# Kernel tuning notes

Measured on AMD Instinct MI355X. Metric: run time of the kernel, lower is better.

The kernel has to match this reference:

```python
import jax, jax.numpy as jnp
import numpy as np
from jax import lax

STRIDE, HID, LAT, R, LVL, SCALE = 8, 128, 64, 3, 4, 4
FF = 50 * 60  # frame_flow spatial size


def bilinear_sample(img, x, y):
    # img: [Q,C,H,W]; x,y: [Q,P] float pixel coords; zero outside image. -> [Q,C,P]
    Q, C, H, W = img.shape
    x0 = jnp.floor(x); y0 = jnp.floor(y)
    wx = x - x0; wy = y - y0
    flat = img.reshape(Q, C, H * W)
    def g(ix, iy):
        valid = (ix >= 0) & (ix <= W - 1) & (iy >= 0) & (iy <= H - 1)
        idx = (jnp.clip(iy, 0, H - 1).astype(jnp.int32) * W
               + jnp.clip(ix, 0, W - 1).astype(jnp.int32))[:, None, :]
        v = jnp.take_along_axis(flat, jnp.broadcast_to(idx, (Q, C, x.shape[-1])), axis=2)
        return v * valid[:, None, :]
    return (g(x0, y0) * ((1 - wy) * (1 - wx))[:, None, :]
            + g(x0 + 1, y0) * ((1 - wy) * wx)[:, None, :]
            + g(x0, y0 + 1) * (wy * (1 - wx))[:, None, :]
            + g(x0 + 1, y0 + 1) * (wy * wx)[:, None, :])


def resize_bilinear(img, oh, ow, align_corners):
    # img: [Q,C,H,W] -> [Q,C,oh,ow], matches F.interpolate(mode='bilinear')
    Q, C, H, W = img.shape
    def coords(o, i):
        if align_corners:
            return jnp.linspace(0.0, i - 1.0, o)
        return jnp.clip((jnp.arange(o) + 0.5) * (i / o) - 0.5, 0.0, i - 1.0)
    ys, xs = coords(oh, H), coords(ow, W)
    y0 = jnp.floor(ys).astype(jnp.int32); y1 = jnp.minimum(y0 + 1, H - 1); wy = ys - y0
    x0 = jnp.floor(xs).astype(jnp.int32); x1 = jnp.minimum(x0 + 1, W - 1); wx = xs - x0
    v = jnp.take(img, y0, axis=2) * (1 - wy)[:, None] + jnp.take(img, y1, axis=2) * wy[:, None]
    return jnp.take(v, x0, axis=3) * (1 - wx) + jnp.take(v, x1, axis=3) * wx


def avg_pool2(x):
    return lax.reduce_window(x, 0.0, lax.add, (1, 1, 2, 2), (1, 1, 2, 2), 'VALID') * 0.25


def encode(x, w, stride):
    # patchify conv + instance-norm (surrogate for BasicEncoder, same in/out shapes)
    y = lax.conv_general_dilated(x, w, (stride, stride), 'VALID',
                                 dimension_numbers=('NCHW', 'OIHW', 'NCHW'))
    m = y.mean(axis=(2, 3), keepdims=True)
    v = y.var(axis=(2, 3), keepdims=True)
    return (y - m) * lax.rsqrt(v + 1e-5)


def build_pyramid(fmaps):
    # fmaps: [B,S,C,H,W] -> list of [B*S,C,Hl,Wl] (CorrBlock.__init__)
    B, S, C, H, W = fmaps.shape
    x = fmaps.reshape(B * S, C, H, W)
    pyr = [x]
    for _ in range(LVL - 1):
        x = avg_pool2(x)
        pyr.append(x)
    return pyr


def corr_pyramid(pyr, feats):
    # feats: [B,S,N,C] -> list of [B*S,N,Hl,Wl] (CorrBlock.corr)
    B, S, N, C = feats.shape
    f = feats.reshape(B * S, N, C)
    scale = 1.0 / jnp.sqrt(jnp.float32(C))
    return [jnp.einsum('qnc,qchw->qnhw', f, p) * scale for p in pyr]


def corr_sample(corrs, coords):
    # CorrBlock.sample: bilinear gather of (2R+1)^2 window per level at coords/2^lvl
    B, S, N, _ = coords.shape
    d = jnp.arange(-R, R + 1, dtype=coords.dtype)
    dy, dx = jnp.meshgrid(d, d, indexing='ij')
    dx = dx.reshape(1, -1); dy = dy.reshape(1, -1)
    out = []
    for i, c in enumerate(corrs):
        H, W = c.shape[-2:]
        cen = coords.reshape(B * S * N, 1, 2) / (2.0 ** i)
        x = cen[..., 0] + dx; y = cen[..., 1] + dy  # [BSN,K]
        v = bilinear_sample(c.reshape(B * S * N, 1, H, W), x, y)
        out.append(v.reshape(B, S, N, -1))
    return jnp.concatenate(out, axis=-1)  # [B,S,N,LVL*(2R+1)^2]


def flows_from(coords):
    B, S, N, _ = coords.shape
    f = (coords[:, 1:] - coords[:, :-1]).transpose(0, 2, 1, 3).reshape(B * N, S - 1, 2)
    return jnp.concatenate([f, f[:, -1:]], axis=1)


def delta_block(fc, fl, ff, xy, w1, b1, w2, b2):
    # surrogate for DeltaBlock / DeltaBlock_temp: MLP over concatenated context
    h = jnp.concatenate([fc, fl, ff, xy], axis=-1)
    return jax.nn.relu(h @ w1 + b1) @ w2 + b2  # [B*N,S,2]


def forward_model(rgbs, points_0, fnet_w, fnet_fine_w, linear_w, linear_b,
                  dbs_w1, dbs_b1, dbs_w2, dbs_b2,
                  dbt_w1, dbt_b1, dbt_w2, dbt_b2, iters):
    B, S, C, H, W = rgbs.shape
    N = points_0.shape[1]
    rgbs = 2.0 * (rgbs / 255.0) - 1.0
    rgbs_ = rgbs.reshape(B * S, C, H, W)
    # frame_flow context (assumes B==1, like the torch code): [N,S,3000]
    ff = jnp.concatenate([rgbs_[-1:, 0], rgbs_[1:, 0] - rgbs_[:-1, 0]], axis=0)[:, None]
    ff = resize_bilinear(ff, 50, 60, False).reshape(1, S, FF)
    frame_flow = jnp.broadcast_to(ff, (N, S, FF))

    # ---- initialize_ : coarse stage (stride 8) ----
    Hc, Wc = H // STRIDE, W // STRIDE
    fmaps_c = encode(rgbs_, fnet_w, STRIDE).reshape(B, S, LAT, Hc, Wc)
    coords = jnp.broadcast_to((points_0 / float(STRIDE))[:, None], (B, S, N, 2))
    f0 = bilinear_sample(fmaps_c[:, 0], coords[:, 0, :, 0], coords[:, 0, :, 1]).transpose(0, 2, 1)
    feats = jnp.broadcast_to(f0[:, None], (B, S, N, LAT))
    xys0_c = jnp.broadcast_to(coords[:, 0].transpose(1, 0, 2), (N, S, 2))
    coords = lax.stop_gradient(coords)
    corrs_c = corr_pyramid(build_pyramid(fmaps_c), feats)
    fc = [resize_bilinear(c, 14, 14, True).reshape(B, S, N, 196) for c in corrs_c]
    fcorrs_ = jnp.stack(fc).mean(0).transpose(0, 2, 1, 3).reshape(B * N, S, 196)
    delta = delta_block(fcorrs_, flows_from(coords), frame_flow, xys0_c,
                        dbs_w1, dbs_b1, dbs_w2, dbs_b2)
    coords = coords + delta.reshape(B, N, S, 2).transpose(0, 2, 1, 3)
    coords_init = coords * float(STRIDE)

    # ---- fine refinement (stride 2), iterative ----
    fs = STRIDE // SCALE  # 2
    Hf, Wf = H // fs, W // fs
    fmaps = encode(rgbs_, fnet_fine_w, fs).reshape(B, S, LAT, Hf, Wf)
    coords = coords_init / float(fs)
    pyr = build_pyramid(fmaps)
    f0 = bilinear_sample(fmaps[:, 0], coords[:, 0, :, 0], coords[:, 0, :, 1]).transpose(0, 2, 1)
    corrs1 = corr_pyramid(pyr, jnp.broadcast_to(f0[:, None], (B, S, N, LAT)))
    xys0 = jnp.broadcast_to(coords[:, 0].transpose(1, 0, 2), (N, S, 2))
    inds2 = jnp.clip(jnp.arange(S) - 2, 0, None)
    inds4 = jnp.clip(jnp.arange(S) - 4, 0, None)
    preds = [coords_init]
    for _ in range(iters):
        coords = lax.stop_gradient(coords)
        def shifted_feats(inds, coords=coords):
            fm = fmaps[:, inds].reshape(B * S, LAT, Hf, Wf)
            co = coords[:, inds].reshape(B * S, N, 2)
            return bilinear_sample(fm, co[..., 0], co[..., 1]).transpose(0, 2, 1).reshape(B, S, N, LAT)
        corrs2 = corr_pyramid(pyr, shifted_feats(inds2))
        corrs4 = corr_pyramid(pyr, shifted_feats(inds4))
        def bn(f):
            return f.transpose(0, 2, 1, 3).reshape(B * N, S, -1)
        fcorrs_ = jnp.concatenate([bn(corr_sample(corrs1, coords)),
                                   bn(corr_sample(corrs2, coords)),
                                   bn(corr_sample(corrs4, coords))], axis=2)
        fcorrs_ = fcorrs_ @ linear_w + linear_b  # 588 -> 392
        delta = delta_block(fcorrs_, flows_from(coords), frame_flow, xys0,
                            dbt_w1, dbt_b1, dbt_w2, dbt_b2)
        coords = coords + delta.reshape(B, N, S, 2).transpose(0, 2, 1, 3)
        preds.append(coords * float(fs))
    return jnp.stack(preds)  # [iters+1, B, S, N, 2]


def setup_inputs():
    ks = jax.random.split(jax.random.key(0), 12)
    B, S, N, H, W = 1, 16, 64, 200, 240
    rgbs = jax.random.uniform(ks[0], (B, S, 1, H, W), jnp.float32) * 255.0
    points_0 = jax.random.uniform(ks[1], (B, N, 2), jnp.float32) * jnp.array([W - 1.0, H - 1.0], jnp.float32)
    d_sp, d_tp = 196 + 2 + FF + 2, 392 + 2 + FF + 2
    return {
        'rgbs': rgbs, 'points_0': points_0,
        'fnet_w': jax.random.normal(ks[2], (LAT, 1, STRIDE, STRIDE), jnp.float32) * 0.1,
        'fnet_fine_w': jax.random.normal(ks[3], (LAT, 1, 2, 2), jnp.float32) * 0.3,
        'linear_w': jax.random.normal(ks[4], (588, 392), jnp.float32) / np.sqrt(588.0).astype(np.float32),
        'linear_b': jnp.zeros((392,), jnp.float32),
        'dbs_w1': jax.random.normal(ks[5], (d_sp, HID), jnp.float32) / np.float32(np.sqrt(d_sp)),
        'dbs_b1': jnp.zeros((HID,), jnp.float32),
        'dbs_w2': jax.random.normal(ks[6], (HID, 2), jnp.float32) / np.float32(np.sqrt(HID)),
        'dbs_b2': jnp.zeros((2,), jnp.float32),
        'dbt_w1': jax.random.normal(ks[7], (d_tp, HID), jnp.float32) / np.float32(np.sqrt(d_tp)),
        'dbt_b1': jnp.zeros((HID,), jnp.float32),
        'dbt_w2': jax.random.normal(ks[8], (HID, 2), jnp.float32) / np.float32(np.sqrt(HID)),
        'dbt_b2': jnp.zeros((2,), jnp.float32),
        'iters': 4,
    }


def reference(rgbs, points_0, fnet_w, fnet_fine_w, linear_w, linear_b,
              dbs_w1, dbs_b1, dbs_w2, dbs_b2,
              dbt_w1, dbt_b1, dbt_w2, dbt_b2, iters):
    return forward_model(rgbs, points_0, fnet_w, fnet_fine_w, linear_w, linear_b,
                         dbs_w1, dbs_b1, dbs_w2, dbs_b2,
                         dbt_w1, dbt_b1, dbt_w2, dbt_b2, iters)
```

## Files before the change

### kernel.cpp

```cpp
#include <hip/hip_runtime.h>

constexpr int cS = 16, cN = 64, cH = 200, cW = 240;
constexpr int cHC = 25, cWC = 30;
constexpr int cHF = 100, cWF = 120;
constexpr int cC = 64;
constexpr int cITERS = 4;
constexpr int cNCH = 50, cCHUNK = 60;

typedef _Float16 half8 __attribute__((ext_vector_type(8)));


__device__ __forceinline__ float bilin_hwc(const float* __restrict__ fm, int Hh, int Ww,
                                           float x, float y, int c) {
  x = fminf(fmaxf(x, -2.0e6f), 2.0e6f);
  y = fminf(fmaxf(y, -2.0e6f), 2.0e6f);
  float x0f = floorf(x), y0f = floorf(y);
  int ix = (int)x0f, iy = (int)y0f;
  float wx = x - x0f, wy = y - y0f;
  float acc = 0.f;
  bool vx0 = (ix >= 0) && (ix < Ww), vx1 = (ix + 1 >= 0) && (ix + 1 < Ww);
  bool vy0 = (iy >= 0) && (iy < Hh), vy1 = (iy + 1 >= 0) && (iy + 1 < Hh);
  if (vy0 && vx0) acc += fm[(iy * Ww + ix) * cC + c] * (1.f - wy) * (1.f - wx);
  if (vy0 && vx1) acc += fm[(iy * Ww + ix + 1) * cC + c] * (1.f - wy) * wx;
  if (vy1 && vx0) acc += fm[((iy + 1) * Ww + ix) * cC + c] * wy * (1.f - wx);
  if (vy1 && vx1) acc += fm[((iy + 1) * Ww + ix + 1) * cC + c] * wy * wx;
  return acc;
}

__device__ __forceinline__ float bilin_raw_h(const _Float16* __restrict__ fm, int Hh, int Ww,
                                             float x, float y, int c, float& wsum) {
  x = fminf(fmaxf(x, -2.0e6f), 2.0e6f);
  y = fminf(fmaxf(y, -2.0e6f), 2.0e6f);
  float x0f = floorf(x), y0f = floorf(y);
  int ix = (int)x0f, iy = (int)y0f;
  float wx = x - x0f, wy = y - y0f;
  float acc = 0.f; wsum = 0.f;
  bool vx0 = (ix >= 0) && (ix < Ww), vx1 = (ix + 1 >= 0) && (ix + 1 < Ww);
  bool vy0 = (iy >= 0) && (iy < Hh), vy1 = (iy + 1 >= 0) && (iy + 1 < Hh);
  float w00 = (1.f - wy) * (1.f - wx), w01 = (1.f - wy) * wx;
  float w10 = wy * (1.f - wx), w11 = wy * wx;
  if (vy0 && vx0) { acc += (float)fm[(iy * Ww + ix) * cC + c] * w00; wsum += w00; }
  if (vy0 && vx1) { acc += (float)fm[(iy * Ww + ix + 1) * cC + c] * w01; wsum += w01; }
  if (vy1 && vx0) { acc += (float)fm[((iy + 1) * Ww + ix) * cC + c] * w10; wsum += w10; }
  if (vy1 && vx1) { acc += (float)fm[((iy + 1) * Ww + ix + 1) * cC + c] * w11; wsum += w11; }
  return acc;
}

constexpr int NB_FFP = 800, NB_CONVC = 1024, NB_CONVF = 1600;

__global__ __launch_bounds__(256) void k_front(const float* __restrict__ rgbs,
                                               const float* __restrict__ w1s,
                                               const float* __restrict__ w1t,
                                               const float* __restrict__ fnw,
                                               const float* __restrict__ fnfw,
                                               float* __restrict__ part,
                                               float* __restrict__ fmc,
                                               _Float16* __restrict__ fmf,
                                               float* __restrict__ partf) {
  __shared__ float smem[512];
  int bid = blockIdx.x, tid = threadIdx.x;
  const float a = 2.0f / 255.0f;

  if (bid < NB_FFP) {
    int s = bid / cNCH, ch = bid % cNCH;
    if (tid < cCHUNK) {
      const float* cur = rgbs + (size_t)s * cH * cW;
      const float* prev = rgbs + (size_t)(s - 1) * cH * cW;
      const float* last = rgbs + (size_t)15 * cH * cW;
      int y = 4 * ch + 1, x = 4 * tid + 1;
      float v = 0.f;
      #pragma unroll
      for (int dy = 0; dy < 2; dy++)
        #pragma unroll
        for (int dx = 0; dx < 2; dx++) {
          int id = (y + dy) * cW + (x + dx);
          float pv = (s == 0) ? (a * last[id] - 1.0f) : (a * (cur[id] - prev[id]));
          v += pv;
        }
      smem[tid] = 0.25f * v;
    }
    __syncthreads();
    int t = tid >> 7, j = tid & 127;
    const float* w = (t == 0) ? (w1s + (size_t)198 * 128) : (w1t + (size_t)394 * 128);
    const float* wr = w + (size_t)ch * cCHUNK * 128 + j;
    float acc = 0.f;
    #pragma unroll 4
    for (int i = 0; i < cCHUNK; i++) acc += smem[i] * wr[(size_t)i * 128];
    part[(((size_t)t * cS + s) * cNCH + ch) * 128 + j] = acc;

  } else if (bid < NB_FFP + NB_CONVC) {
    int idx = bid - NB_FFP;
    int q = idx >> 6, c = idx & 63;
    float* wl = smem;
    float* red = smem + 64;
    if (tid < 64) wl[tid] = fnw[c * 64 + tid];
    __syncthreads();
    const float* img = rgbs + (size_t)q * cH * cW;
    float vals[3];
    float sum = 0.f, ss = 0.f;
    #pragma unroll
    for (int i = 0; i < 3; i++) {
      int pos = tid + i * 256;
      float v = 0.f;
      if (pos < 750) {
        int y = pos / cWC, x = pos % cWC;
        const float* base = img + (y * 8) * cW + x * 8;
        float acc = 0.f, wsum = 0.f;
        for (int ky = 0; ky < 8; ky++)
          #pragma unroll
          for (int kx = 0; kx < 8; kx++) {
            float wv = wl[ky * 8 + kx];
            acc += wv * base[ky * cW + kx];
            wsum += wv;
          }
        v = a * acc - wsum;
        sum += v; ss += v * v;
      }
      vals[i] = v;
    }
    red[tid] = sum; __syncthreads();
    for (int st = 128; st > 0; st >>= 1) { if (tid < st) red[tid] += red[tid + st]; __syncthreads(); }
    float tsum = red[0]; __syncthreads();
    red[tid] = ss; __syncthreads();
    for (int st = 128; st > 0; st >>= 1) { if (tid < st) red[tid] += red[tid + st]; __syncthreads(); }
    float tss = red[0];
    float mean = tsum / 750.0f;
    float var = tss / 750.0f - mean * mean;
    float rstd = rsqrtf(var + 1e-5f);
    #pragma unroll
    for (int i = 0; i < 3; i++) {
      int pos = tid + i * 256;
      if (pos < 750) fmc[((size_t)q * 750 + pos) * cC + c] = (vals[i] - mean) * rstd;
    }

  } else {
    int idx = bid - NB_FFP - NB_CONVC;
    int q = idx / cHF, y = idx % cHF;
    int lane = tid & 63, wv = tid >> 6;
    float w0 = fnfw[lane * 4 + 0], w1 = fnfw[lane * 4 + 1];
    float w2 = fnfw[lane * 4 + 2], w3 = fnfw[lane * 4 + 3];
    float wsum = w0 + w1 + w2 + w3;
    const float* img = rgbs + (size_t)q * cH * cW;
    float sum = 0.f, ss = 0.f;
    for (int x = wv; x < cWF; x += 4) {
      const float* b = img + (2 * y) * cW + 2 * x;
      float v = a * (w0 * b[0] + w1 * b[1] + w2 * b[cW] + w3 * b[cW + 1]) - wsum;
      fmf[(((size_t)q * cHF + y) * cWF + x) * cC + lane] = (_Float16)v;
      sum += v; ss += v * v;
    }
    float* red = smem;
    red[(0 * 4 + wv) * 64 + lane] = sum;
    red[(1 * 4 + wv) * 64 + lane] = ss;
    __syncthreads();
    if (wv == 0) {
      float s4 = red[0 * 64 + lane] + red[1 * 64 + lane] + red[2 * 64 + lane] + red[3 * 64 + lane];
      float q4 = red[(4 + 0) * 64 + lane] + red[(4 + 1) * 64 + lane] +
                 red[(4 + 2) * 64 + lane] + red[(4 + 3) * 64 + lane];
      size_t o = ((size_t)q * cHF + y) * 64 + lane;
      partf[o * 2 + 0] = s4;
      partf[o * 2 + 1] = q4;
    }
  }
}

__global__ __launch_bounds__(256) void k_mid(const float* __restrict__ part,
                                             float* __restrict__ ffw_s, float* __restrict__ ffw_t,
                                             const float* __restrict__ lw, const float* __restrict__ lb,
                                             const float* __restrict__ w1t, const float* __restrict__ b1t,
                                             _Float16* __restrict__ LWc, float* __restrict__ b1te,
                                             const float* __restrict__ partf, float* __restrict__ stats,
                                             const float* __restrict__ fmc, float* __restrict__ arp) {
  __shared__ float smem[14784];
  int bid = blockIdx.x, tid = threadIdx.x;

  if (bid < 16) {
    int s = bid, t = tid >> 7, j = tid & 127;
    const float* p = part + (((size_t)t * cS + s) * cNCH) * 128 + j;
    float acc = 0.f;
    for (int c = 0; c < cNCH; c++) acc += p[(size_t)c * 128];
    ((t == 0) ? ffw_s : ffw_t)[s * 128 + j] = acc;

  } else if (bid < 91) {
    int b2 = bid - 16, g = tid >> 7, j = tid & 127;
    if (b2 < 74) {
      int k0 = b2 * 8 + g * 4;
      if (k0 < 588) {
        const float* l0 = lw + (size_t)(k0 + 0) * 392;
        const float* l1 = lw + (size_t)(k0 + 1) * 392;
        const float* l2 = lw + (size_t)(k0 + 2) * 392;
        const float* l3 = lw + (size_t)(k0 + 3) * 392;
        float a0 = 0.f, a1 = 0.f, a2 = 0.f, a3 = 0.f;
        for (int m = 0; m < 392; m++) {
          float wv = w1t[(size_t)m * 128 + j];
          a0 += l0[m] * wv; a1 += l1[m] * wv; a2 += l2[m] * wv; a3 += l3[m] * wv;
        }
        LWc[(size_t)(k0 + 0) * 128 + j] = (_Float16)a0;
        LWc[(size_t)(k0 + 1) * 128 + j] = (_Float16)a1;
        LWc[(size_t)(k0 + 2) * 128 + j] = (_Float16)a2;
        LWc[(size_t)(k0 + 3) * 128 + j] = (_Float16)a3;
      }
    } else if (g == 0) {
      float acc = b1t[j];
      for (int m = 0; m < 392; m++) acc += lb[m] * w1t[(size_t)m * 128 + j];
      b1te[j] = acc;
    }

  } else if (bid < 107) {
    int q = bid - 91, c = tid & 63, g = tid >> 6;
    float s0 = 0.f, s1 = 0.f;
    for (int yy = 0; yy < 25; yy++) {
      size_t o = ((size_t)q * cHF + g * 25 + yy) * 64 + c;
      s0 += partf[o * 2 + 0];
      s1 += partf[o * 2 + 1];
    }
    smem[g * 64 + c] = s0;
    smem[256 + g * 64 + c] = s1;
    __syncthreads();
    if (g == 0) {
      stats[(q * 64 + c) * 2 + 0] = smem[c] + smem[64 + c] + smem[128 + c] + smem[192 + c];
      stats[(q * 64 + c) * 2 + 1] = smem[256 + c] + smem[320 + c] + smem[384 + c] + smem[448 + c];
    }

  } else {
    int q = bid - 107;
    float* pc1 = smem;
    float* pc2 = smem + 11520;
    float* pc3 = smem + 14208;
    const float* L0 = fmc + (size_t)q * 750 * cC;
    for (int i = tid; i < 12 * 15 * 64; i += 256) {
      int c = i & 63, pos = i >> 6, oy = pos / 15, ox = pos % 15;
      const float* b = L0 + ((2 * oy) * 30 + 2 * ox) * cC + c;
      pc1[i] = 0.25f * (b[0] + b[cC] + b[30 * cC] + b[30 * cC + cC]);
    }
    __syncthreads();
    for (int i = tid; i < 6 * 7 * 64; i += 256) {
      int c = i & 63, pos = i >> 6, oy = pos / 7, ox = pos % 7;
      const float* b = pc1 + ((2 * oy) * 15 + 2 * ox) * cC + c;
      pc2[i] = 0.25f * (b[0] + b[cC] + b[15 * cC] + b[15 * cC + cC]);
    }
    __syncthreads();
    for (int i = tid; i < 3 * 3 * 64; i += 256) {
      int c = i & 63, pos = i >> 6, oy = pos / 3, ox = pos % 3;
      const float* b = pc2 + ((2 * oy) * 7 + 2 * ox) * cC + c;
      pc3[i] = 0.25f * (b[0] + b[cC] + b[7 * cC] + b[7 * cC + cC]);
    }
    __syncthreads();
    const int Hs[4] = {25, 12, 6, 3}, Ws[4] = {30, 15, 7, 3};
    for (int i = tid; i < 196 * 64; i += 256) {
      int c = i & 63, pos = i >> 6, o = pos / 14, p = pos % 14;
      float acc = 0.f;
      #pragma unroll
      for (int l = 0; l < 4; l++) {
        float yy = (float)(o * (Hs[l] - 1)) / 13.0f;
        float xx = (float)(p * (Ws[l] - 1)) / 13.0f;
        int y0 = (int)floorf(yy); int y1 = min(y0 + 1, Hs[l] - 1); float wy = yy - (float)y0;
        int x0 = (int)floorf(xx); int x1 = min(x0 + 1, Ws[l] - 1); float wx = xx - (float)x0;
        const float* L = (l == 0) ? L0 : ((l == 1) ? pc1 : ((l == 2) ? pc2 : pc3));
        float v00 = L[(y0 * Ws[l] + x0) * cC + c], v01 = L[(y0 * Ws[l] + x1) * cC + c];
        float v10 = L[(y1 * Ws[l] + x0) * cC + c], v11 = L[(y1 * Ws[l] + x1) * cC + c];
        acc += (v00 * (1.f - wy) + v10 * wy) * (1.f - wx) + (v01 * (1.f - wy) + v11 * wy) * wx;
      }
      arp[((size_t)q * 196 + pos) * cC + c] = acc * 0.25f * 0.125f;
    }
  }
}

__global__ __launch_bounds__(256) void k_mix(const float* __restrict__ arp, const float* __restrict__ fmc,
                                             const float* __restrict__ w1, const float* __restrict__ b1,
                                             const float* __restrict__ ffw, const float* __restrict__ w2,
                                             const float* __restrict__ b2, const float* __restrict__ pts,
                                             float* __restrict__ cof, float* __restrict__ xys,
                                             float* __restrict__ out,
                                             const _Float16* __restrict__ fmf,
                                             _Float16* __restrict__ pf1, _Float16* __restrict__ pf2,
                                             _Float16* __restrict__ pf3) {
  __shared__ __align__(16) unsigned char smemraw[38400];
  int bid = blockIdx.x, tid = threadIdx.x;

  if (bid < 256) {
    int n = bid >> 2, sb = (bid & 3) * 4;
    float* fc = (float*)smemraw;
    float* f0l = fc + 784;
    float* hp = f0l + 64;
    float* hl = hp + 1024;
    float xx = pts[n * 2 + 0] * 0.125f, yy = pts[n * 2 + 1] * 0.125f;
    if (tid < 64) f0l[tid] = bilin_hwc(fmc, cHC, cWC, xx, yy, tid);
    __syncthreads();
    for (int i = tid; i < 784; i += 256) {
      int r = i / 196, k = i - r * 196;
      const float4* b4 = (const float4*)(arp + ((size_t)(sb + r) * 196 + k) * cC);
      float acc = 0.f;
      #pragma unroll
      for (int c4 = 0; c4 < 16; c4++) {
        float4 v = b4[c4];
        acc += v.x * f0l[c4 * 4 + 0] + v.y * f0l[c4 * 4 + 1] +
               v.z * f0l[c4 * 4 + 2] + v.w * f0l[c4 * 4 + 3];
      }
      fc[i] = acc;
    }
    __syncthreads();
    int j = tid & 127, half = tid >> 7;
    float h0 = 0.f, h1 = 0.f, h2 = 0.f, h3 = 0.f;
    int k0 = half * 98;
    for (int k = k0; k < k0 + 98; k++) {
      float wv = w1[(size_t)k * 128 + j];
      h0 += fc[0 * 196 + k] * wv; h1 += fc[1 * 196 + k] * wv;
      h2 += fc[2 * 196 + k] * wv; h3 += fc[3 * 196 + k] * wv;
    }
    hp[(half * 4 + 0) * 128 + j] = h0; hp[(half * 4 + 1) * 128 + j] = h1;
    hp[(half * 4 + 2) * 128 + j] = h2; hp[(half * 4 + 3) * 128 + j] = h3;
    __syncthreads();
    if (half == 0) {
      const float* Wxy = w1 + (size_t)3198 * 128;
      #pragma unroll
      for (int r = 0; r < 4; r++) {
        int s = sb + r;
        float v = hp[r * 128 + j] + hp[(4 + r) * 128 + j] + b1[j] +
                  ffw[s * 128 + j] + xx * Wxy[j] + yy * Wxy[128 + j];
        hl[r * 128 + j] = fmaxf(v, 0.f);
      }
    }
    __syncthreads();
    if (tid < 8) {
      int r = tid >> 1, d = tid & 1;
      float acc = b2[d];
      for (int k = 0; k < 128; k++) acc += hl[r * 128 + k] * w2[k * 2 + d];
      int s = sb + r;
      float cc = pts[n * 2 + d] * 0.125f + acc;
      out[((size_t)s * cN + n) * 2 + d] = cc * 8.0f;
      cof[((size_t)s * cN + n) * 2 + d] = cc * 4.0f;
      if (s == 0) xys[n * 2 + d] = cc * 4.0f;
    }

  } else {
    int u = bid - 256;
    int q = u / 13, b = u % 13;
    _Float16* l1 = (_Float16*)smemraw;
    _Float16* l2 = l1 + 15360;
    int nr1 = (b == 12) ? 2 : 4;
    const _Float16* F = fmf + (size_t)q * cHF * cWF * cC;
    for (int i = tid; i < nr1 * 60 * 64; i += 256) {
      int c = i & 63, pos = i >> 6, rl = pos / 60, ox = pos % 60;
      int r1 = 4 * b + rl;
      const _Float16* p = F + ((size_t)(2 * r1) * cWF + 2 * ox) * cC + c;
      float v = 0.25f * ((float)p[0] + (float)p[cC] + (float)p[cWF * cC] + (float)p[cWF * cC + cC]);
      _Float16 h = (_Float16)v;
      l1[i] = h;
      pf1[(((size_t)q * 50 + r1) * 60 + ox) * cC + c] = h;
    }
    __syncthreads();
    int nr2 = (b == 12) ? 1 : 2;
    for (int i = tid; i < nr2 * 30 * 64; i += 256) {
      int c = i & 63, pos = i >> 6, rl = pos / 30, ox = pos % 30;
      const _Float16* p = l1 + ((2 * rl) * 60 + 2 * ox) * 64 + c;
      float v = 0.25f * ((float)p[0] + (float)p[64] + (float)p[60 * 64] + (float)p[60 * 64 + 64]);
      _Float16 h = (_Float16)v;
      l2[i] = h;
      pf2[(((size_t)q * 25 + 2 * b + rl) * 30 + ox) * cC + c] = h;
    }
    __syncthreads();
    if (b < 12) {
      for (int i = tid; i < 15 * 64; i += 256) {
        int c = i & 63, ox = i >> 6;
        const _Float16* p = l2 + (2 * ox) * 64 + c;
        float v = 0.25f * ((float)p[0] + (float)p[64] + (float)p[30 * 64] + (float)p[30 * 64 + 64]);
        pf3[(((size_t)q * 12 + b) * 15 + ox) * cC + c] = (_Float16)v;
      }
    }
  }
}

__global__ __launch_bounds__(256) void k_iter(const _Float16* __restrict__ p0, const _Float16* __restrict__ p1,
                                              const _Float16* __restrict__ p2, const _Float16* __restrict__ p3,
                                              const float* __restrict__ stats,
                                              const _Float16* __restrict__ LWc, const float* __restrict__ b1e,
                                              const float* __restrict__ ffw, const float* __restrict__ w1t,
                                              const float* __restrict__ w2, const float* __restrict__ b2,
                                              const float* __restrict__ cof_cur, float* __restrict__ cof_nxt,
                                              const float* __restrict__ xys, float* __restrict__ out) {
  int bid = blockIdx.x;
  int w = (bid & 7) * 128 + (bid >> 3);
  int s = w >> 6, n = w & 63;
  __shared__ float feat2[3][64];
  __shared__ float biasS[3];
  __shared__ float fcL[588];
  __shared__ float hp[2][128];
  __shared__ float hl[128];
  int tid = threadIdx.x;

  {
    int t = tid >> 6, c = tid & 63;
    if (t < 3) {
      float sS = stats[(s * 64 + c) * 2 + 0], qS = stats[(s * 64 + c) * 2 + 1];
      float meanS = sS / 12000.f, varS = qS / 12000.f - meanS * meanS;
      float rstdS = rsqrtf(varS + 1e-5f);
      int ssrc = (t == 0) ? 0 : max(s - 2 * t, 0);
      float fx, fy;
      if (t == 0) { fx = xys[n * 2 + 0]; fy = xys[n * 2 + 1]; }
      else {
        fx = cof_cur[((size_t)ssrc * cN + n) * 2 + 0];
        fy = cof_cur[((size_t)ssrc * cN + n) * 2 + 1];
      }
      float s2 = stats[(ssrc * 64 + c) * 2 + 0], q2 = stats[(ssrc * 64 + c) * 2 + 1];
      float m2 = s2 / 12000.f, v2 = q2 / 12000.f - m2 * m2;
      float r2 = rsqrtf(v2 + 1e-5f);
      float ws;
      float raw = bilin_raw_h(p0 + (size_t)ssrc * cHF * cWF * cC, cHF, cWF, fx, fy, c, ws);
      float featn = (raw - m2 * ws) * r2;
      feat2[t][c] = featn * rstdS * 0.125f;
      float bc = featn * (-meanS * rstdS) * 0.125f;
      #pragma unroll
      for (int o = 32; o; o >>= 1) bc += __shfl_xor(bc, o);
      if (c == 0) biasS[t] = bc;
    }
  }
  __syncthreads();

  {
    int l = tid >> 6, lane = tid & 63;
    const _Float16* Ls[4] = {p0, p1, p2, p3};
    const int Hs[4] = {cHF, 50, 25, 12}, Ws[4] = {cWF, 60, 30, 15};
    float cx = cof_cur[((size_t)s * cN + n) * 2 + 0];
    float cy = cof_cur[((size_t)s * cN + n) * 2 + 1];
    float sc = 1.0f / (float)(1 << l);
    float x = fminf(fmaxf(cx * sc, -2.0e6f), 2.0e6f);
    float y = fminf(fmaxf(cy * sc, -2.0e6f), 2.0e6f);
    float x0f = floorf(x), y0f = floorf(y);
    float wx = x - x0f, wy = y - y0f;
    int dxi = lane & 7, dyi = lane >> 3;
    int ix = (int)x0f + dxi - 3, iy = (int)y0f + dyi - 3;
    int Hl = Hs[l], Wl = Ws[l];
    float d[3] = {0.f, 0.f, 0.f};
    if (ix >= 0 && ix < Wl && iy >= 0 && iy < Hl) {
      const _Float16* row = Ls[l] + (((size_t)s * Hl + iy) * Wl + ix) * cC;
      float a0 = 0.f, a1 = 0.f, a2 = 0.f;
      #pragma unroll
      for (int c8 = 0; c8 < 8; c8++) {
        half8 v = *(const half8*)(row + c8 * 8);
        #pragma unroll
        for (int e = 0; e < 8; e++) {
          float f = (float)v[e];
          a0 += f * feat2[0][c8 * 8 + e];
          a1 += f * feat2[1][c8 * 8 + e];
          a2 += f * feat2[2][c8 * 8 + e];
        }
      }
      d[0] = a0 + biasS[0]; d[1] = a1 + biasS[1]; d[2] = a2 + biasS[2];
    }
    int dy = lane / 7, dx = lane - dy * 7;
    int bb = (lane < 49) ? (dy * 8 + dx) : 0;
    float w00 = (1.f - wy) * (1.f - wx), w01 = (1.f - wy) * wx;
    float w10 = wy * (1.f - wx), w11 = wy * wx;
    #pragma unroll
    for (int t = 0; t < 3; t++) {
      float d00 = __shfl(d[t], bb, 64);
      float d01 = __shfl(d[t], bb + 1, 64);
      float d10 = __shfl(d[t], bb + 8, 64);
      float d11 = __shfl(d[t], bb + 9, 64);
      if (lane < 49)
        fcL[t * 196 + l * 49 + lane] = w00 * d00 + w01 * d01 + w10 * d10 + w11 * d11;
    }
  }
  __syncthreads();

  int j = tid & 127, half = tid >> 7;
  {
    float h = 0.f;
    int k0 = half * 294;
    const _Float16* Lw = LWc + (size_t)k0 * 128 + j;
    for (int k = 0; k < 294; k++) h += fcL[k0 + k] * (float)Lw[(size_t)k * 128];
    hp[half][j] = h;
  }
  __syncthreads();
  if (half == 0) {
    const float* Wfl = w1t + (size_t)392 * 128;
    const float* Wxy = w1t + (size_t)3394 * 128;
    float xx = xys[n * 2 + 0], yy = xys[n * 2 + 1];
    int sA = min(s + 1, 15), sB = (s == 15) ? 14 : s;
    float flx = cof_cur[(sA * cN + n) * 2 + 0] - cof_cur[(sB * cN + n) * 2 + 0];
    float fly = cof_cur[(sA * cN + n) * 2 + 1] - cof_cur[(sB * cN + n) * 2 + 1];
    float v = hp[0][j] + hp[1][j] + b1e[j] + ffw[s * 128 + j] +
              flx * Wfl[j] + fly * Wfl[128 + j] + xx * Wxy[j] + yy * Wxy[128 + j];
    hl[j] = fmaxf(v, 0.f);
  }
  __syncthreads();
  if (tid < 2) {
    int d = tid;
    float acc = b2[d];
    for (int k = 0; k < 128; k++) acc += hl[k] * w2[k * 2 + d];
    float cc = cof_cur[((size_t)s * cN + n) * 2 + d] + acc;
    cof_nxt[((size_t)s * cN + n) * 2 + d] = cc;
    out[((size_t)s * cN + n) * 2 + d] = cc * 2.0f;
  }
}

extern "C" void kernel_launch(void* const* d_in, const int* in_sizes, int n_in,
                              void* d_out, int out_size, void* d_ws, size_t ws_size,
                              hipStream_t stream) {
  (void)in_sizes; (void)n_in; (void)out_size; (void)ws_size;
  const float* rgbs = (const float*)d_in[0];
  const float* pts  = (const float*)d_in[1];
  const float* fnw  = (const float*)d_in[2];
  const float* fnfw = (const float*)d_in[3];
  const float* lw   = (const float*)d_in[4];
  const float* lb   = (const float*)d_in[5];
  const float* w1s  = (const float*)d_in[6];
  const float* b1s  = (const float*)d_in[7];
  const float* w2s  = (const float*)d_in[8];
  const float* b2s  = (const float*)d_in[9];
  const float* w1t  = (const float*)d_in[10];
  const float* b1t  = (const float*)d_in[11];
  const float* w2t  = (const float*)d_in[12];
  const float* b2t  = (const float*)d_in[13];
  float* out = (float*)d_out;

  float* p = (float*)d_ws;
  auto alloc = [&](size_t nf) { float* r = p; p += nf; return r; };
  float* part  = alloc((size_t)2 * cS * cNCH * 128);
  float* ffw_s = alloc(cS * 128);
  float* ffw_t = alloc(cS * 128);
  _Float16* LWc = (_Float16*)alloc((size_t)588 * 128 / 2);
  float* b1te  = alloc(128);
  float* fmc   = alloc((size_t)cS * cHC * cWC * cC);
  float* arp   = alloc((size_t)cS * 196 * cC);
  float* partf = alloc((size_t)cS * cHF * cC * 2);
  float* stats = alloc(cS * cC * 2);
  _Float16* fmf = (_Float16*)alloc((size_t)cS * cHF * cWF * cC / 2);
  _Float16* pf1 = (_Float16*)alloc((size_t)cS * 50 * 60 * cC / 2);
  _Float16* pf2 = (_Float16*)alloc((size_t)cS * 25 * 30 * cC / 2);
  _Float16* pf3 = (_Float16*)alloc((size_t)cS * 12 * 15 * cC / 2);
  float* xys0  = alloc(cN * 2);
  float* cofA  = alloc((size_t)cS * cN * 2);
  float* cofB  = alloc((size_t)cS * cN * 2);

  k_front<<<NB_FFP + NB_CONVC + NB_CONVF, 256, 0, stream>>>(
      rgbs, w1s, w1t, fnw, fnfw, part, fmc, fmf, partf);
  k_mid<<<123, 256, 0, stream>>>(part, ffw_s, ffw_t, lw, lb, w1t, b1t, LWc, b1te,
                                 partf, stats, fmc, arp);
  k_mix<<<464, 256, 0, stream>>>(arp, fmc, w1s, b1s, ffw_s, w2s, b2s, pts,
                                 cofA, xys0, out, fmf, pf1, pf2, pf3);
  float* cbuf[2] = {cofA, cofB};
  for (int it = 0; it < cITERS; it++) {
    float* cur = cbuf[it & 1];
    float* nxt = cbuf[(it & 1) ^ 1];
    k_iter<<<1024, 256, 0, stream>>>(fmf, pf1, pf2, pf3, stats, LWc, b1te, ffw_t,
                                     w1t, w2t, b2t, cur, nxt, xys0,
                                     out + (size_t)(it + 1) * cS * cN * 2);
  }
}
```

Before: 172.4 us.

## Restructure coarse encoder conv, defer instance-norm, and use fp16 dot2 in iterations

The coarse patchify conv now runs one block per image row, caching the image strip and transposed weights in shared memory. It writes unnormalized fp16 features plus partial statistics, and a new k_mid block reduces those into per-channel stats. Normalization is folded algebraically into k_mix by scaling the sampled feature and adding a bias term. In k_iter, the correlation dot products and the MLP inner loop switch to packed fp16 fdot2 with pair-packed weights, which cuts conversions and ALU work at some cost in precision.

Result: no change. 173.0 us (+0.3%).

```diff
diff --git a/kernel.cpp b/kernel.cpp
--- a/kernel.cpp
+++ b/kernel.cpp
@@ -8,24 +8,8 @@
 constexpr int cNCH = 50, cCHUNK = 60;
 
 typedef _Float16 half8 __attribute__((ext_vector_type(8)));
-
-
-__device__ __forceinline__ float bilin_hwc(const float* __restrict__ fm, int Hh, int Ww,
-                                           float x, float y, int c) {
-  x = fminf(fmaxf(x, -2.0e6f), 2.0e6f);
-  y = fminf(fmaxf(y, -2.0e6f), 2.0e6f);
-  float x0f = floorf(x), y0f = floorf(y);
-  int ix = (int)x0f, iy = (int)y0f;
-  float wx = x - x0f, wy = y - y0f;
-  float acc = 0.f;
-  bool vx0 = (ix >= 0) && (ix < Ww), vx1 = (ix + 1 >= 0) && (ix + 1 < Ww);
-  bool vy0 = (iy >= 0) && (iy < Hh), vy1 = (iy + 1 >= 0) && (iy + 1 < Hh);
-  if (vy0 && vx0) acc += fm[(iy * Ww + ix) * cC + c] * (1.f - wy) * (1.f - wx);
-  if (vy0 && vx1) acc += fm[(iy * Ww + ix + 1) * cC + c] * (1.f - wy) * wx;
-  if (vy1 && vx0) acc += fm[((iy + 1) * Ww + ix) * cC + c] * wy * (1.f - wx);
-  if (vy1 && vx1) acc += fm[((iy + 1) * Ww + ix + 1) * cC + c] * wy * wx;
-  return acc;
-}
+typedef _Float16 h2 __attribute__((ext_vector_type(2)));
+
 
 __device__ __forceinline__ float bilin_raw_h(const _Float16* __restrict__ fm, int Hh, int Ww,
                                              float x, float y, int c, float& wsum) {
@@ -46,7 +30,7 @@
   return acc;
 }
 
-constexpr int NB_FFP = 800, NB_CONVC = 1024, NB_CONVF = 1600;
+constexpr int NB_FFP = 800, NB_CONVC = 400, NB_CONVF = 1600;
 
 __global__ __launch_bounds__(256) void k_front(const float* __restrict__ rgbs,
                                                const float* __restrict__ w1s,
@@ -54,10 +38,11 @@
                                                const float* __restrict__ fnw,
                                                const float* __restrict__ fnfw,
                                                float* __restrict__ part,
-                                               float* __restrict__ fmc,
+                                               _Float16* __restrict__ fmc,
+                                               float* __restrict__ partc,
                                                _Float16* __restrict__ fmf,
                                                float* __restrict__ partf) {
-  __shared__ float smem[512];
+  __shared__ float smem[6528];
   int bid = blockIdx.x, tid = threadIdx.x;
   const float a = 2.0f / 255.0f;
 
@@ -90,47 +75,42 @@
 
   } else if (bid < NB_FFP + NB_CONVC) {
     int idx = bid - NB_FFP;
-    int q = idx >> 6, c = idx & 63;
-    float* wl = smem;
-    float* red = smem + 64;
-    if (tid < 64) wl[tid] = fnw[c * 64 + tid];
-    __syncthreads();
-    const float* img = rgbs + (size_t)q * cH * cW;
-    float vals[3];
+    int q = idx / 25, y = idx % 25;
+    float* imgL = smem;
+    float* wlT = smem + 1920;
+    float* red = smem + 6016;
+    const float* img = rgbs + ((size_t)q * cH + y * 8) * cW;
+    for (int i = tid; i < 1920; i += 256) imgL[i] = img[i];
+    for (int i = tid; i < 4096; i += 256) {
+      int tap = i >> 6, c = i & 63;
+      wlT[i] = fnw[c * 64 + tap];
+    }
+    __syncthreads();
+    int c = tid & 63, g = tid >> 6;
+    float wsum = 0.f;
+    for (int t = 0; t < 64; t++) wsum += wlT[t * 64 + c];
     float sum = 0.f, ss = 0.f;
-    #pragma unroll
-    for (int i = 0; i < 3; i++) {
-      int pos = tid + i * 256;
-      float v = 0.f;
-      if (pos < 750) {
-        int y = pos / cWC, x = pos % cWC;
-        const float* base = img + (y * 8) * cW + x * 8;
-        float acc = 0.f, wsum = 0.f;
-        for (int ky = 0; ky < 8; ky++)
-          #pragma unroll
-          for (int kx = 0; kx < 8; kx++) {
-            float wv = wl[ky * 8 + kx];
-            acc += wv * base[ky * cW + kx];
-            wsum += wv;
-          }
-        v = a * acc - wsum;
-        sum += v; ss += v * v;
-      }
-      vals[i] = v;
-    }
-    red[tid] = sum; __syncthreads();
-    for (int st = 128; st > 0; st >>= 1) { if (tid < st) red[tid] += red[tid + st]; __syncthreads(); }
-    float tsum = red[0]; __syncthreads();
-    red[tid] = ss; __syncthreads();
-    for (int st = 128; st > 0; st >>= 1) { if (tid < st) red[tid] += red[tid + st]; __syncthreads(); }
-    float tss = red[0];
-    float mean = tsum / 750.0f;
-    float var = tss / 750.0f - mean * mean;
-    float rstd = rsqrtf(var + 1e-5f);
-    #pragma unroll
-    for (int i = 0; i < 3; i++) {
-      int pos = tid + i * 256;
-      if (pos < 750) fmc[((size_t)q * 750 + pos) * cC + c] = (vals[i] - mean) * rstd;
+    for (int x = g; x < 30; x += 4) {
+      float acc = 0.f;
+      #pragma unroll
+      for (int ky = 0; ky < 8; ky++)
+        #pragma unroll
+        for (int kx = 0; kx < 8; kx++)
+          acc += wlT[(ky * 8 + kx) * 64 + c] * imgL[ky * 240 + x * 8 + kx];
+      float v = a * acc - wsum;
+      fmc[((size_t)q * 750 + y * 30 + x) * cC + c] = (_Float16)v;
+      sum += v; ss += v * v;
+    }
+    red[(0 * 4 + g) * 64 + c] = sum;
+    red[(1 * 4 + g) * 64 + c] = ss;
+    __syncthreads();
+    if (g == 0) {
+      float s4 = red[0 * 64 + c] + red[1 * 64 + c] + red[2 * 64 + c] + red[3 * 64 + c];
+      float q4 = red[(4 + 0) * 64 + c] + red[(4 + 1) * 64 + c] +
+                 red[(4 + 2) * 64 + c] + red[(4 + 3) * 64 + c];
+      size_t o = ((size_t)q * 25 + y) * 64 + c;
+      partc[o * 2 + 0] = s4;
+      partc[o * 2 + 1] = q4;
     }
 
   } else {
@@ -167,9 +147,10 @@
                                              float* __restrict__ ffw_s, float* __restrict__ ffw_t,
                                              const float* __restrict__ lw, const float* __restrict__ lb,
                                              const float* __restrict__ w1t, const float* __restrict__ b1t,
-                                             _Float16* __restrict__ LWc, float* __restrict__ b1te,
+                                             h2* __restrict__ LWc2, float* __restrict__ b1te,
                                              const float* __restrict__ partf, float* __restrict__ stats,
-                                             const float* __restrict__ fmc, float* __restrict__ arp) {
+                                             const float* __restrict__ partc, float* __restrict__ statc,
+                                             const _Float16* __restrict__ fmc, float* __restrict__ arp) {
   __shared__ float smem[14784];
   int bid = blockIdx.x, tid = threadIdx.x;
 
@@ -194,10 +175,9 @@
           float wv = w1t[(size_t)m * 128 + j];
           a0 += l0[m] * wv; a1 += l1[m] * wv; a2 += l2[m] * wv; a3 += l3[m] * wv;
         }
-        LWc[(size_t)(k0 + 0) * 128 + j] = (_Float16)a0;
-        LWc[(size_t)(k0 + 1) * 128 + j] = (_Float16)a1;
-        LWc[(size_t)(k0 + 2) * 128 + j] = (_Float16)a2;
-        LWc[(size_t)(k0 + 3) * 128 + j] = (_Float16)a3;
+        int kk = k0 >> 1;
+        LWc2[(size_t)(kk + 0) * 128 + j] = h2{(_Float16)a0, (_Float16)a1};
+        LWc2[(size_t)(kk + 1) * 128 + j] = h2{(_Float16)a2, (_Float16)a3};
       }
     } else if (g == 0) {
       float acc = b1t[j];
@@ -221,16 +201,32 @@
       stats[(q * 64 + c) * 2 + 1] = smem[256 + c] + smem[320 + c] + smem[384 + c] + smem[448 + c];
     }
 
+  } else if (bid < 123) {
+    int q = bid - 107, c = tid & 63, g = tid >> 6;
+    float s0 = 0.f, s1 = 0.f;
+    for (int yy = g; yy < 25; yy += 4) {
+      size_t o = ((size_t)q * 25 + yy) * 64 + c;
+      s0 += partc[o * 2 + 0];
+      s1 += partc[o * 2 + 1];
+    }
+    smem[g * 64 + c] = s0;
+    smem[256 + g * 64 + c] = s1;
+    __syncthreads();
+    if (g == 0) {
+      statc[(q * 64 + c) * 2 + 0] = smem[c] + smem[64 + c] + smem[128 + c] + smem[192 + c];
+      statc[(q * 64 + c) * 2 + 1] = smem[256 + c] + smem[320 + c] + smem[384 + c] + smem[448 + c];
+    }
+
   } else {
-    int q = bid - 107;
+    int q = bid - 123;
     float* pc1 = smem;
     float* pc2 = smem + 11520;
     float* pc3 = smem + 14208;
-    const float* L0 = fmc + (size_t)q * 750 * cC;
+    const _Float16* L0 = fmc + (size_t)q * 750 * cC;
     for (int i = tid; i < 12 * 15 * 64; i += 256) {
       int c = i & 63, pos = i >> 6, oy = pos / 15, ox = pos % 15;
-      const float* b = L0 + ((2 * oy) * 30 + 2 * ox) * cC + c;
-      pc1[i] = 0.25f * (b[0] + b[cC] + b[30 * cC] + b[30 * cC + cC]);
+      const _Float16* b = L0 + ((2 * oy) * 30 + 2 * ox) * cC + c;
+      pc1[i] = 0.25f * ((float)b[0] + (float)b[cC] + (float)b[30 * cC] + (float)b[30 * cC + cC]);
     }
     __syncthreads();
     for (int i = tid; i < 6 * 7 * 64; i += 256) {
@@ -255,9 +251,16 @@
         float xx = (float)(p * (Ws[l] - 1)) / 13.0f;
         int y0 = (int)floorf(yy); int y1 = min(y0 + 1, Hs[l] - 1); float wy = yy - (float)y0;
         int x0 = (int)floorf(xx); int x1 = min(x0 + 1, Ws[l] - 1); float wx = xx - (float)x0;
-        const float* L = (l == 0) ? L0 : ((l == 1) ? pc1 : ((l == 2) ? pc2 : pc3));
-        float v00 = L[(y0 * Ws[l] + x0) * cC + c], v01 = L[(y0 * Ws[l] + x1) * cC + c];
-        float v10 = L[(y1 * Ws[l] + x0) * cC + c], v11 = L[(y1 * Ws[l] + x1) * cC + c];
+        float v00, v01, v10, v11;
+        if (l == 0) {
+          v00 = (float)L0[(y0 * 30 + x0) * cC + c]; v01 = (float)L0[(y0 * 30 + x1) * cC + c];
+          v10 = (float)L0[(y1 * 30 + x0) * cC + c]; v11 = (float)L0[(y1 * 30 + x1) * cC + c];
+        } else {
+          const float* L = (l == 1) ? pc1 : ((l == 2) ? pc2 : pc3);
+          int Wl = Ws[l];
+          v00 = L[(y0 * Wl + x0) * cC + c]; v01 = L[(y0 * Wl + x1) * cC + c];
+          v10 = L[(y1 * Wl + x0) * cC + c]; v11 = L[(y1 * Wl + x1) * cC + c];
+        }
         acc += (v00 * (1.f - wy) + v10 * wy) * (1.f - wx) + (v01 * (1.f - wy) + v11 * wy) * wx;
       }
       arp[((size_t)q * 196 + pos) * cC + c] = acc * 0.25f * 0.125f;
@@ -265,7 +268,8 @@
   }
 }
 
-__global__ __launch_bounds__(256) void k_mix(const float* __restrict__ arp, const float* __restrict__ fmc,
+__global__ __launch_bounds__(256) void k_mix(const float* __restrict__ arp, const _Float16* __restrict__ fmc,
+                                             const float* __restrict__ statc,
                                              const float* __restrict__ w1, const float* __restrict__ b1,
                                              const float* __restrict__ ffw, const float* __restrict__ w2,
                                              const float* __restrict__ b2, const float* __restrict__ pts,
@@ -280,35 +284,59 @@
   if (bid < 256) {
     int n = bid >> 2, sb = (bid & 3) * 4;
     float* fc = (float*)smemraw;
-    float* f0l = fc + 784;
-    float* hp = f0l + 64;
+    float* f0n = fc + 784;
+    float* featc = f0n + 64;
+    float* biasc = featc + 256;
+    float* hp = biasc + 4;
     float* hl = hp + 1024;
     float xx = pts[n * 2 + 0] * 0.125f, yy = pts[n * 2 + 1] * 0.125f;
-    if (tid < 64) f0l[tid] = bilin_hwc(fmc, cHC, cWC, xx, yy, tid);
+    if (tid < 64) {
+      float ws;
+      float raw = bilin_raw_h(fmc, cHC, cWC, xx, yy, tid, ws);
+      float mu = statc[tid * 2 + 0] / 750.f;
+      float var = statc[tid * 2 + 1] / 750.f - mu * mu;
+      float r0 = rsqrtf(var + 1e-5f);
+      f0n[tid] = r0 * (raw - mu * ws);
+    }
+    __syncthreads();
+    {
+      int rr = tid >> 6, c = tid & 63;
+      int s = sb + rr;
+      float mu = statc[(s * 64 + c) * 2 + 0] / 750.f;
+      float var = statc[(s * 64 + c) * 2 + 1] / 750.f - mu * mu;
+      float rs = rsqrtf(var + 1e-5f);
+      float fv = rs * f0n[c];
+      featc[rr * 64 + c] = fv;
+      float bc = -0.25f * 0.125f * mu * fv;
+      #pragma unroll
+      for (int o = 32; o; o >>= 1) bc += __shfl_xor(bc, o);
+      if (c == 0) biasc[rr] = bc;
+    }
     __syncthreads();
     for (int i = tid; i < 784; i += 256) {
       int r = i / 196, k = i - r * 196;
       const float4* b4 = (const float4*)(arp + ((size_t)(sb + r) * 196 + k) * cC);
+      const float* fv = featc + r * 64;
       float acc = 0.f;
       #pragma unroll
       for (int c4 = 0; c4 < 16; c4++) {
         float4 v = b4[c4];
-        acc += v.x * f0l[c4 * 4 + 0] + v.y * f0l[c4 * 4 + 1] +
-               v.z * f0l[c4 * 4 + 2] + v.w * f0l[c4 * 4 + 3];
-      }
-      fc[i] = acc;
+        acc += v.x * fv[c4 * 4 + 0] + v.y * fv[c4 * 4 + 1] +
+               v.z * fv[c4 * 4 + 2] + v.w * fv[c4 * 4 + 3];
+      }
+      fc[i] = acc + biasc[r];
     }
     __syncthreads();
     int j = tid & 127, half = tid >> 7;
-    float h0 = 0.f, h1 = 0.f, h2 = 0.f, h3 = 0.f;
+    float h0 = 0.f, h1 = 0.f, h2v = 0.f, h3 = 0.f;
     int k0 = half * 98;
     for (int k = k0; k < k0 + 98; k++) {
       float wv = w1[(size_t)k * 128 + j];
       h0 += fc[0 * 196 + k] * wv; h1 += fc[1 * 196 + k] * wv;
-      h2 += fc[2 * 196 + k] * wv; h3 += fc[3 * 196 + k] * wv;
+      h2v += fc[2 * 196 + k] * wv; h3 += fc[3 * 196 + k] * wv;
     }
     hp[(half * 4 + 0) * 128 + j] = h0; hp[(half * 4 + 1) * 128 + j] = h1;
-    hp[(half * 4 + 2) * 128 + j] = h2; hp[(half * 4 + 3) * 128 + j] = h3;
+    hp[(half * 4 + 2) * 128 + j] = h2v; hp[(half * 4 + 3) * 128 + j] = h3;
     __syncthreads();
     if (half == 0) {
       const float* Wxy = w1 + (size_t)3198 * 128;
@@ -373,7 +401,7 @@
 __global__ __launch_bounds__(256) void k_iter(const _Float16* __restrict__ p0, const _Float16* __restrict__ p1,
                                               const _Float16* __restrict__ p2, const _Float16* __restrict__ p3,
                                               const float* __restrict__ stats,
-                                              const _Float16* __restrict__ LWc, const float* __restrict__ b1e,
+                                              const h2* __restrict__ LWc2, const float* __restrict__ b1e,
                                               const float* __restrict__ ffw, const float* __restrict__ w1t,
                                               const float* __restrict__ w2, const float* __restrict__ b2,
                                               const float* __restrict__ cof_cur, float* __restrict__ cof_nxt,
@@ -381,9 +409,9 @@
   int bid = blockIdx.x;
   int w = (bid & 7) * 128 + (bid >> 3);
   int s = w >> 6, n = w & 63;
-  __shared__ float feat2[3][64];
+  __shared__ _Float16 feat2h[3][64];
   __shared__ float biasS[3];
-  __shared__ float fcL[588];
+  __shared__ _Float16 fcL16[588];
   __shared__ float hp[2][128];
   __shared__ float hl[128];
   int tid = threadIdx.x;
@@ -407,7 +435,7 @@
       float ws;
       float raw = bilin_raw_h(p0 + (size_t)ssrc * cHF * cWF * cC, cHF, cWF, fx, fy, c, ws);
       float featn = (raw - m2 * ws) * r2;
-      feat2[t][c] = featn * rstdS * 0.125f;
+      feat2h[t][c] = (_Float16)(featn * rstdS * 0.125f);
       float bc = featn * (-meanS * rstdS) * 0.125f;
       #pragma unroll
       for (int o = 32; o; o >>= 1) bc += __shfl_xor(bc, o);
@@ -420,6 +448,9 @@
     int l = tid >> 6, lane = tid & 63;
     const _Float16* Ls[4] = {p0, p1, p2, p3};
     const int Hs[4] = {cHF, 50, 25, 12}, Ws[4] = {cWF, 60, 30, 15};
+    const h2* fh0 = (const h2*)feat2h[0];
+    const h2* fh1 = (const h2*)feat2h[1];
+    const h2* fh2 = (const h2*)feat2h[2];
     float cx = cof_cur[((size_t)s * cN + n) * 2 + 0];
     float cy = cof_cur[((size_t)s * cN + n) * 2 + 1];
     float sc = 1.0f / (float)(1 << l);
@@ -438,11 +469,11 @@
       for (int c8 = 0; c8 < 8; c8++) {
         half8 v = *(const half8*)(row + c8 * 8);
         #pragma unroll
-        for (int e = 0; e < 8; e++) {
-          float f = (float)v[e];
-          a0 += f * feat2[0][c8 * 8 + e];
-          a1 += f * feat2[1][c8 * 8 + e];
-          a2 += f * feat2[2][c8 * 8 + e];
+        for (int e2 = 0; e2 < 4; e2++) {
+          h2 pv = {v[e2 * 2], v[e2 * 2 + 1]};
+          a0 = __builtin_amdgcn_fdot2(pv, fh0[c8 * 4 + e2], a0, false);
+          a1 = __builtin_amdgcn_fdot2(pv, fh1[c8 * 4 + e2], a1, false);
+          a2 = __builtin_amdgcn_fdot2(pv, fh2[c8 * 4 + e2], a2, false);
         }
       }
       d[0] = a0 + biasS[0]; d[1] = a1 + biasS[1]; d[2] = a2 + biasS[2];
@@ -458,17 +489,20 @@
       float d10 = __shfl(d[t], bb + 8, 64);
       float d11 = __shfl(d[t], bb + 9, 64);
       if (lane < 49)
-        fcL[t * 196 + l * 49 + lane] = w00 * d00 + w01 * d01 + w10 * d10 + w11 * d11;
+        fcL16[t * 196 + l * 49 + lane] = (_Float16)(w00 * d00 + w01 * d01 + w10 * d10 + w11 * d11);
     }
   }
   __syncthreads();
 
   int j = tid & 127, half = tid >> 7;
   {
+    const h2* fcl2 = (const h2*)fcL16;
     float h = 0.f;
-    int k0 = half * 294;
-    const _Float16* Lw = LWc + (size_t)k0 * 128 + j;
-    for (int k = 0; k < 294; k++) h += fcL[k0 + k] * (float)Lw[(size_t)k * 128];
+    int kk0 = half * 147;
+    const h2* Lw = LWc2 + (size_t)kk0 * 128 + j;
+    #pragma unroll 4
+    for (int kk = 0; kk < 147; kk++)
+      h = __builtin_amdgcn_fdot2(fcl2[kk0 + kk], Lw[(size_t)kk * 128], h, false);
     hp[half][j] = h;
   }
   __syncthreads();
@@ -519,9 +553,11 @@
   float* part  = alloc((size_t)2 * cS * cNCH * 128);
   float* ffw_s = alloc(cS * 128);
   float* ffw_t = alloc(cS * 128);
-  _Float16* LWc = (_Float16*)alloc((size_t)588 * 128 / 2);
+  h2* LWc2     = (h2*)alloc((size_t)588 * 128 / 2);
   float* b1te  = alloc(128);
-  float* fmc   = alloc((size_t)cS * cHC * cWC * cC);
+  _Float16* fmc = (_Float16*)alloc((size_t)cS * 750 * cC / 2);
+  float* partc = alloc((size_t)cS * 25 * cC * 2);
+  float* statc = alloc(cS * cC * 2);
   float* arp   = alloc((size_t)cS * 196 * cC);
   float* partf = alloc((size_t)cS * cHF * cC * 2);
   float* stats = alloc(cS * cC * 2);
@@ -534,16 +570,16 @@
   float* cofB  = alloc((size_t)cS * cN * 2);
 
   k_front<<<NB_FFP + NB_CONVC + NB_CONVF, 256, 0, stream>>>(
-      rgbs, w1s, w1t, fnw, fnfw, part, fmc, fmf, partf);
-  k_mid<<<123, 256, 0, stream>>>(part, ffw_s, ffw_t, lw, lb, w1t, b1t, LWc, b1te,
-                                 partf, stats, fmc, arp);
-  k_mix<<<464, 256, 0, stream>>>(arp, fmc, w1s, b1s, ffw_s, w2s, b2s, pts,
+      rgbs, w1s, w1t, fnw, fnfw, part, fmc, partc, fmf, partf);
+  k_mid<<<139, 256, 0, stream>>>(part, ffw_s, ffw_t, lw, lb, w1t, b1t, LWc2, b1te,
+                                 partf, stats, partc, statc, fmc, arp);
+  k_mix<<<464, 256, 0, stream>>>(arp, fmc, statc, w1s, b1s, ffw_s, w2s, b2s, pts,
                                  cofA, xys0, out, fmf, pf1, pf2, pf3);
   float* cbuf[2] = {cofA, cofB};
   for (int it = 0; it < cITERS; it++) {
     float* cur = cbuf[it & 1];
     float* nxt = cbuf[(it & 1) ^ 1];
-    k_iter<<<1024, 256, 0, stream>>>(fmf, pf1, pf2, pf3, stats, LWc, b1te, ffw_t,
+    k_iter<<<1024, 256, 0, stream>>>(fmf, pf1, pf2, pf3, stats, LWc2, b1te, ffw_t,
                                      w1t, w2t, b2t, cur, nxt, xys0,
                                      out + (size_t)(it + 1) * cS * cN * 2);
   }
```
